# Performance work log

Measured on AMD Instinct MI355X. Metric: run time of the kernel, lower is better.

## Reference

```python
import jax, jax.numpy as jnp
import numpy as np

NEG_SLOPE = 0.01  # torch leaky_relu default


def kan_linear(x, coeffs, bias):
    """Fourier KAN linear. x: [..., I], coeffs: [2, O, I, G], bias: [O] or None."""
    G = coeffs.shape[-1]
    k = jnp.arange(1, G + 1, dtype=x.dtype)            # [G]
    xb = x[..., None] * k                               # [..., I, G]
    y = jnp.einsum('...ig,oig->...o', jnp.cos(xb), coeffs[0]) \
      + jnp.einsum('...ig,oig->...o', jnp.sin(xb), coeffs[1])
    if bias is not None:
        y = y + bias
    return y


def setup_inputs() -> dict:
    key = jax.random.key(0)
    N, E = 50000, 500000
    IN, IE, FN, FE, H, G = 128, 64, 128, 32, 4, 4
    D = IN + IE
    HFE, HFN = H * FE, H * FN
    ks = jax.random.split(key, 16)
    def nrm(k, shape, scale):
        return jax.random.normal(k, shape, dtype=jnp.float32) * scale
    return {
        'node_feats': nrm(ks[0], (N, IN), 1.0),
        'edge_feats': nrm(ks[1], (E, IE), 1.0),
        'src': jax.random.randint(ks[2], (E,), 0, N, dtype=jnp.int32),
        'dst': jax.random.randint(ks[3], (E,), 0, N, dtype=jnp.int32),
        'W_ni': nrm(ks[4], (IN, HFE), 0.05),
        'W_nj': nrm(ks[5], (IN, HFE), 0.05),
        'W_fij': nrm(ks[6], (IE, HFE), 0.05),
        'W_node': nrm(ks[7], (D, HFN), 0.05),
        'b_node': jnp.zeros((HFN,), jnp.float32),
        'attn': nrm(ks[8], (H, FE), 0.1),
        'bias_edge': jnp.zeros((HFE,), jnp.float32),
        'ek_c': nrm(ks[9], (2, HFE, HFE, 1), 1.0 / np.sqrt(HFE)),
        'ek_b': jnp.zeros((HFE,), jnp.float32),
        'nk_c': nrm(ks[10], (2, D, D, 1), 1.0 / np.sqrt(D)),
        'nk_b': jnp.zeros((D,), jnp.float32),
        'on_c': nrm(ks[11], (2, FN, FN, G), 1.0 / np.sqrt(FN * G)),
        'on_b': jnp.zeros((FN,), jnp.float32),
        'oe_c': nrm(ks[12], (2, FE, FE, G), 1.0 / np.sqrt(FE * G)),
        'oe_b': jnp.zeros((FE,), jnp.float32),
    }


def reference(node_feats, edge_feats, src, dst, W_ni, W_nj, W_fij, W_node, b_node,
              attn, bias_edge, ek_c, ek_b, nk_c, nk_b, on_c, on_b, oe_c, oe_b):
    N = node_feats.shape[0]
    H, FE = attn.shape

    # edge feature path: f_ni[u] + f_nj[v] + f_fij -> KAN -> bias -> leaky_relu
    f = (node_feats @ W_ni)[src] + (node_feats @ W_nj)[dst] + edge_feats @ W_fij  # [E, H*FE]
    f = kan_linear(f, ek_c, ek_b) + bias_edge
    f = jax.nn.leaky_relu(f, NEG_SLOPE)
    f = f.reshape(-1, H, FE)                                  # [E, H, FE]

    # attention scores + edge softmax over incoming edges of dst
    scores = jnp.sum(f * attn, axis=-1)                        # [E, H]
    smax = jax.ops.segment_max(scores, dst, num_segments=N)    # [N, H]
    e = jnp.exp(scores - smax[dst])
    ssum = jax.ops.segment_sum(e, dst, num_segments=N)
    a = e / ssum[dst]                                          # [E, H]

    # mean aggregation of raw edge feats onto dst nodes
    ones = jnp.ones((src.shape[0],), node_feats.dtype)
    deg = jax.ops.segment_sum(ones, dst, num_segments=N)       # [N]
    agg = jax.ops.segment_sum(edge_feats, dst, num_segments=N) / jnp.maximum(deg, 1.0)[:, None]

    merged = jnp.concatenate([node_feats, agg], axis=1)        # [N, IN+IE]
    merged = kan_linear(merged, nk_c, nk_b)

    h = (merged @ W_node + b_node).reshape(N, H, -1)           # [N, H, FN]
    m = h[src] * a[:, :, None]                                 # [E, H, FN]
    h_out = jax.ops.segment_sum(m, dst, num_segments=N)        # [N, H, FN]
    h_out = jnp.sum(jax.nn.leaky_relu(h_out, NEG_SLOPE), axis=1)  # [N, FN]

    f_sum = jnp.sum(f, axis=1)                                 # [E, FE]
    out_node = kan_linear(h_out, on_c, on_b)                   # [N, FN]
    out_edge = kan_linear(f_sum, oe_c, oe_b)                   # [E, FE]
    return out_node, out_edge
```

## Files before the change

### kernel.cpp

```cpp
#include <hip/hip_runtime.h>
#include <hip/hip_bf16.h>
#include <math.h>

#define NEG 0.01f

typedef __attribute__((ext_vector_type(8))) short short8;
typedef __attribute__((ext_vector_type(4))) float f32x4;
typedef unsigned short ushort;

#define MFMA(a,b,c) __builtin_amdgcn_mfma_f32_16x16x32_bf16(a,b,c,0,0,0)

__device__ __forceinline__ float leaky(float x){ return x >= 0.f ? x : NEG*x; }
__device__ __forceinline__ ushort b16(float f){
  unsigned int u = __float_as_uint(f);
  unsigned int r = (u + 0x7FFF + ((u >> 16) & 1)) >> 16;
  return (ushort)r;
}

__global__ void k_deg(const int* __restrict__ dst, int* __restrict__ deg, int E){
  int e = blockIdx.x*256 + threadIdx.x;
  if (e < E) atomicAdd(&deg[dst[e]], 1);
}

__global__ __launch_bounds__(1024) void k_scan(const int* __restrict__ deg, int* __restrict__ off, int N){
  __shared__ int buf[1024];
  __shared__ int carry_s;
  if (threadIdx.x == 0) carry_s = 0;
  __syncthreads();
  for (int base = 0; base < N; base += 1024){
    int i = base + threadIdx.x;
    int v = (i < N) ? deg[i] : 0;
    buf[threadIdx.x] = v;
    __syncthreads();
    for (int s = 1; s < 1024; s <<= 1){
      int t = (threadIdx.x >= s) ? buf[threadIdx.x - s] : 0;
      __syncthreads();
      buf[threadIdx.x] += t;
      __syncthreads();
    }
    if (i < N) off[i] = carry_s + buf[threadIdx.x] - v;
    int tot = buf[1023];
    __syncthreads();
    if (threadIdx.x == 0) carry_s += tot;
    __syncthreads();
  }
  if (threadIdx.x == 0) off[N] = carry_s;
}

__global__ void k_fill(const int* __restrict__ dst, const int* __restrict__ off,
                       int* __restrict__ cursor, int* __restrict__ eids, int E){
  int e = blockIdx.x*256 + threadIdx.x;
  if (e < E){
    int d = dst[e];
    int p = atomicAdd(&cursor[d], 1);
    eids[off[d] + p] = e;
  }
}

__global__ void k_prep2(const float* __restrict__ W_ni, const float* __restrict__ W_nj,
                        const float* __restrict__ W_fij, const float* __restrict__ W_node,
                        const float* __restrict__ ek_c, const float* __restrict__ nk_c,
                        const float* __restrict__ on_c, const float* __restrict__ oe_c,
                        ushort* __restrict__ Bni, ushort* __restrict__ Bnj,
                        ushort* __restrict__ Bfij, ushort* __restrict__ BE,
                        ushort* __restrict__ BN_, ushort* __restrict__ BW,
                        ushort* __restrict__ BO, ushort* __restrict__ BOE){
  int t = blockIdx.x*256 + threadIdx.x;
  if (t < 16384){ int o = t >> 7, i = t & 127; Bni[t] = b16(W_ni[i*128 + o]); return; }
  t -= 16384;
  if (t < 16384){ int o = t >> 7, i = t & 127; Bnj[t] = b16(W_nj[i*128 + o]); return; }
  t -= 16384;
  if (t < 8192){ int o = t >> 6, i = t & 63; Bfij[t] = b16(W_fij[i*128 + o]); return; }
  t -= 8192;
  if (t < 32768){ int o = t >> 8, k = t & 255; int tt = k >> 7, i = k & 127;
    BE[t] = b16(ek_c[((tt*128 + o) << 7) + i]); return; }
  t -= 32768;
  if (t < 73728){ int o = t / 384, k = t % 384; int tt = (k >= 192), i = k - tt*192;
    BN_[t] = b16(nk_c[(tt*192 + o)*192 + i]); return; }
  t -= 73728;
  if (t < 98304){ int o = t / 192, i = t % 192; BW[t] = b16(W_node[i*512 + o]); return; }
  t -= 98304;
  if (t < 131072){ int o = t >> 10, k = t & 1023; int tt = k >> 9, q = k & 511, i = q >> 2, g = q & 3;
    BO[t] = b16(on_c[(((tt*128 + o) << 7) + i)*4 + g]); return; }
  t -= 131072;
  if (t < 8192){ int o = t >> 8, k = t & 255; int tt = k >> 7, q = k & 127, i = q >> 2, g = q & 3;
    BOE[t] = b16(oe_c[((tt*32 + o)*32 + i)*4 + g]); return; }
}

template<int MODE>
__global__ __launch_bounds__(256) void k_mm(
    const float* __restrict__ A, int lda, const float* __restrict__ A2,
    const ushort* __restrict__ B,
    float* __restrict__ C, int ldc, const float* __restrict__ bias,
    int M, int K)
{
  __shared__ __align__(16) ushort As[64*40];
  const int tid = threadIdx.x;
  const int lane = tid & 63, w = tid >> 6;
  const int l15 = lane & 15, kg = lane >> 4;
  const int r0 = blockIdx.x * 64;
  const int c0 = blockIdx.y * 64;
  const int rg = (w & 1) * 2;
  const int cgb = (w >> 1) * 2;
  f32x4 acc[2][2] = {};
  const int srow = tid >> 2;
  const int kk = (tid & 3) * 8;

  for (int k0 = 0; k0 < K; k0 += 32){
    {
      int row = r0 + srow;
      ushort v[8];
      if (MODE == 0){
        if (row < M){
          const float* p = A + (size_t)row*lda + k0 + kk;
          float4 a = *(const float4*)p, b = *(const float4*)(p+4);
          v[0]=b16(a.x); v[1]=b16(a.y); v[2]=b16(a.z); v[3]=b16(a.w);
          v[4]=b16(b.x); v[5]=b16(b.y); v[6]=b16(b.z); v[7]=b16(b.w);
        } else { for (int j=0;j<8;j++) v[j]=0; }
      } else if (MODE == 1){
        int k = k0 + kk;
        int tt = k >> 9, i = (k & 511) >> 2;
        float x0 = 0.f, x1 = 0.f;
        if (row < M){ x0 = A[(size_t)row*128 + i]; x1 = A[(size_t)row*128 + i + 1]; }
        #pragma unroll
        for (int g = 1; g <= 4; g++){
          v[g-1]   = b16(tt ? __sinf(x0*(float)g) : __cosf(x0*(float)g));
          v[3+g]   = b16(tt ? __sinf(x1*(float)g) : __cosf(x1*(float)g));
        }
      } else {
        int k = k0 + kk;
        int tt = (k >= 192), i = k - tt*192;
        float xv8[8] = {0,0,0,0,0,0,0,0};
        if (row < M){
          const float* sp = (i < 128) ? (A + (size_t)row*128 + i) : (A2 + (size_t)row*64 + (i - 128));
          float4 a = *(const float4*)sp, b = *(const float4*)(sp+4);
          xv8[0]=a.x; xv8[1]=a.y; xv8[2]=a.z; xv8[3]=a.w;
          xv8[4]=b.x; xv8[5]=b.y; xv8[6]=b.z; xv8[7]=b.w;
        }
        #pragma unroll
        for (int j = 0; j < 8; j++)
          v[j] = b16(tt ? __sinf(xv8[j]) : __cosf(xv8[j]));
      }
      *(short8*)&As[srow*40 + kk] = *(short8*)v;
    }
    __syncthreads();
    short8 afr[2], bfr[2];
    #pragma unroll
    for (int q = 0; q < 2; q++)
      afr[q] = *(const short8*)&As[((rg+q)*16 + l15)*40 + kg*8];
    #pragma unroll
    for (int q = 0; q < 2; q++)
      bfr[q] = *(const short8*)(B + (size_t)(c0 + (cgb+q)*16 + l15)*K + k0 + kg*8);
    #pragma unroll
    for (int i = 0; i < 2; i++)
      #pragma unroll
      for (int j = 0; j < 2; j++)
        acc[i][j] = MFMA(afr[i], bfr[j], acc[i][j]);
    __syncthreads();
  }
  #pragma unroll
  for (int i = 0; i < 2; i++){
    #pragma unroll
    for (int j = 0; j < 2; j++){
      int col = c0 + (cgb+j)*16 + l15;
      float bv = bias ? bias[col] : 0.f;
      #pragma unroll
      for (int r = 0; r < 4; r++){
        int row = r0 + (rg+i)*16 + kg*4 + r;
        if (row < M) C[(size_t)row*ldc + col] = acc[i][j][r] + bv;
      }
    }
  }
}

__global__ __launch_bounds__(256) void k_edge(
    const float* __restrict__ P,
    const float* __restrict__ ef,
    const int* __restrict__ src, const int* __restrict__ dst,
    const ushort* __restrict__ Bfij,
    const ushort* __restrict__ BE,
    const ushort* __restrict__ BOE,
    const float* __restrict__ ek_b, const float* __restrict__ bias_edge,
    const float* __restrict__ attn, const float* __restrict__ oe_b,
    float* __restrict__ scores,
    float* __restrict__ out_edge,
    int E)
{
  __shared__ __align__(16) ushort cs[32*264];
  __shared__ float fsum[32*33];
  __shared__ float attn_s[128], ekb_s[128], oeb_s[32];
  __shared__ int se[32], de[32];
  const int tid = threadIdx.x;
  const int lane = tid & 63, w = tid >> 6;
  const int l15 = lane & 15, kg = lane >> 4;
  const int e0 = blockIdx.x << 5;

  if (tid < 128){ attn_s[tid] = attn[tid]; ekb_s[tid] = ek_b[tid] + bias_edge[tid]; }
  if (tid < 32){ oeb_s[tid] = oe_b[tid]; se[tid] = src[e0+tid]; de[tid] = dst[e0+tid]; }
  __syncthreads();

  const int eg = w & 1, cq = w >> 1;

  short8 afe[2];
  #pragma unroll
  for (int ks = 0; ks < 2; ks++){
    const float* p = ef + (size_t)(e0 + eg*16 + l15)*64 + ks*32 + kg*8;
    float4 u0 = *(const float4*)p, u1 = *(const float4*)(p+4);
    ushort tv[8] = {b16(u0.x),b16(u0.y),b16(u0.z),b16(u0.w),b16(u1.x),b16(u1.y),b16(u1.z),b16(u1.w)};
    afe[ks] = *(short8*)tv;
  }
  float xv[4][4];
  #pragma unroll
  for (int cg = 0; cg < 4; cg++){
    int c = (cq*4 + cg)*16;
    f32x4 acc = {0.f,0.f,0.f,0.f};
    #pragma unroll
    for (int ks = 0; ks < 2; ks++){
      short8 bf = *(const short8*)(Bfij + (size_t)(c + l15)*64 + ks*32 + kg*8);
      acc = MFMA(afe[ks], bf, acc);
    }
    int col = c + l15;
    #pragma unroll
    for (int r = 0; r < 4; r++){
      int e = eg*16 + kg*4 + r;
      xv[cg][r] = acc[r] + P[(size_t)se[e]*256 + col] + P[(size_t)de[e]*256 + 128 + col];
    }
  }
  #pragma unroll
  for (int cg = 0; cg < 4; cg++){
    int col = (cq*4 + cg)*16 + l15;
    #pragma unroll
    for (int r = 0; r < 4; r++){
      int e = eg*16 + kg*4 + r;
      cs[e*264 + col]       = b16(__cosf(xv[cg][r]));
      cs[e*264 + 128 + col] = b16(__sinf(xv[cg][r]));
    }
  }
  __syncthreads();

  short8 af[8];
  #pragma unroll
  for (int ks = 0; ks < 8; ks++)
    af[ks] = *(const short8*)&cs[(eg*16 + l15)*264 + ks*32 + kg*8];
  float fv[4][4];
  #pragma unroll
  for (int cg = 0; cg < 4; cg++){
    int c = (cq*4 + cg)*16;
    f32x4 acc = {0.f,0.f,0.f,0.f};
    #pragma unroll
    for (int ks = 0; ks < 8; ks++){
      short8 bf = *(const short8*)(BE + (size_t)(c + l15)*256 + ks*32 + kg*8);
      acc = MFMA(af[ks], bf, acc);
    }
    int col = c + l15;
    #pragma unroll
    for (int r = 0; r < 4; r++)
      fv[cg][r] = leaky(acc[r] + ekb_s[col]);
  }
  __syncthreads();
  float* f_lds = (float*)cs;
  #pragma unroll
  for (int cg = 0; cg < 4; cg++){
    int col = (cq*4 + cg)*16 + l15;
    #pragma unroll
    for (int r = 0; r < 4; r++)
      f_lds[(eg*16 + kg*4 + r)*132 + col] = fv[cg][r];
  }
  __syncthreads();

  if (tid < 128){
    int e = tid >> 2, h = tid & 3;
    float s = 0.f;
    #pragma unroll
    for (int j = 0; j < 32; j++) s += f_lds[e*132 + h*32 + j] * attn_s[h*32 + j];
    scores[(size_t)(e0 + e)*4 + h] = s;
  }
  {
    int e = tid >> 3, j0 = (tid & 7)*4;
    #pragma unroll
    for (int j2 = 0; j2 < 4; j2++){
      int j = j0 + j2;
      fsum[e*33 + j] = f_lds[e*132 + j] + f_lds[e*132 + 32 + j]
                     + f_lds[e*132 + 64 + j] + f_lds[e*132 + 96 + j];
    }
  }
  __syncthreads();

  {
    int e = tid >> 3, i0 = (tid & 7)*4;
    ushort cb[16], sb[16];
    #pragma unroll
    for (int i2 = 0; i2 < 4; i2++){
      float x = fsum[e*33 + i0 + i2];
      #pragma unroll
      for (int g = 1; g <= 4; g++){
        float xg = x * (float)g;
        cb[i2*4 + g - 1] = b16(__cosf(xg));
        sb[i2*4 + g - 1] = b16(__sinf(xg));
      }
    }
    *(short8*)&cs[e*264 + i0*4]           = ((short8*)cb)[0];
    *(short8*)&cs[e*264 + i0*4 + 8]       = ((short8*)cb)[1];
    *(short8*)&cs[e*264 + 128 + i0*4]     = ((short8*)sb)[0];
    *(short8*)&cs[e*264 + 128 + i0*4 + 8] = ((short8*)sb)[1];
  }
  __syncthreads();

  {
    int eg5 = w & 1, cg5 = w >> 1;
    f32x4 acc = {0.f,0.f,0.f,0.f};
    #pragma unroll
    for (int ks = 0; ks < 8; ks++){
      short8 a  = *(const short8*)&cs[(eg5*16 + l15)*264 + ks*32 + kg*8];
      short8 bf = *(const short8*)(BOE + (size_t)(cg5*16 + l15)*256 + ks*32 + kg*8);
      acc = MFMA(a, bf, acc);
    }
    int col = cg5*16 + l15;
    #pragma unroll
    for (int r = 0; r < 4; r++){
      int e = eg5*16 + kg*4 + r;
      out_edge[(size_t)(e0 + e)*32 + col] = acc[r] + oeb_s[col];
    }
  }
}

__global__ __launch_bounds__(256) void k_nodestats(
    const float* __restrict__ edge_feats, const float* __restrict__ scores,
    const int* __restrict__ off, const int* __restrict__ eids,
    float* __restrict__ agg, float* __restrict__ smax, float* __restrict__ rssum, int N)
{
  int n = blockIdx.x*4 + (threadIdx.x >> 6);
  int lane = threadIdx.x & 63;
  if (n >= N) return;
  int s0 = off[n], s1 = off[n+1], d = s1 - s0;
  float acc = 0.f;
  for (int t = s0; t < s1; t++){
    int eid = eids[t];
    acc += edge_feats[(size_t)eid*64 + lane];
  }
  agg[(size_t)n*64 + lane] = acc / (float)max(d, 1);
  if (lane < 4){
    float m = -1e30f;
    for (int t = s0; t < s1; t++) m = fmaxf(m, scores[(size_t)eids[t]*4 + lane]);
    float ss = 0.f;
    for (int t = s0; t < s1; t++) ss += __expf(scores[(size_t)eids[t]*4 + lane] - m);
    smax[n*4 + lane]  = (d > 0) ? m : 0.f;
    rssum[n*4 + lane] = (d > 0) ? 1.f/ss : 0.f;
  }
}

__global__ __launch_bounds__(256) void k_aggr(
    const float* __restrict__ h,
    const float* __restrict__ scores,
    const int* __restrict__ src,
    const int* __restrict__ off, const int* __restrict__ eids,
    const float* __restrict__ smax, const float* __restrict__ rssum,
    float* __restrict__ h_out, int N)
{
  __shared__ float part[256];
  int n = blockIdx.x;
  int tid = threadIdx.x;
  int ha = tid >> 7;
  int s0 = off[n], s1 = off[n+1];
  float ma = smax[n*4 + ha],  mb = smax[n*4 + ha + 2];
  float ra = rssum[n*4 + ha], rb = rssum[n*4 + ha + 2];
  float acc_a = 0.f, acc_b = 0.f;
  for (int t = s0; t < s1; t++){
    int eid = eids[t];
    int sv = src[eid];
    float aa = __expf(scores[(size_t)eid*4 + ha]     - ma) * ra;
    float ab = __expf(scores[(size_t)eid*4 + ha + 2] - mb) * rb;
    acc_a += aa * h[(size_t)sv*512 + tid];
    acc_b += ab * h[(size_t)sv*512 + 256 + tid];
  }
  part[tid] = leaky(acc_a) + leaky(acc_b);
  __syncthreads();
  if (tid < 128) h_out[(size_t)n*128 + tid] = part[tid] + part[tid + 128];
}

extern "C" void kernel_launch(void* const* d_in, const int* in_sizes, int n_in,
                              void* d_out, int out_size, void* d_ws, size_t ws_size,
                              hipStream_t stream){
  const float* node_feats = (const float*)d_in[0];
  const float* edge_feats = (const float*)d_in[1];
  const int*   src        = (const int*)  d_in[2];
  const int*   dst        = (const int*)  d_in[3];
  const float* W_ni       = (const float*)d_in[4];
  const float* W_nj       = (const float*)d_in[5];
  const float* W_fij      = (const float*)d_in[6];
  const float* W_node     = (const float*)d_in[7];
  const float* b_node     = (const float*)d_in[8];
  const float* attn       = (const float*)d_in[9];
  const float* bias_edge  = (const float*)d_in[10];
  const float* ek_c       = (const float*)d_in[11];
  const float* ek_b       = (const float*)d_in[12];
  const float* nk_c       = (const float*)d_in[13];
  const float* nk_b       = (const float*)d_in[14];
  const float* on_c       = (const float*)d_in[15];
  const float* on_b       = (const float*)d_in[16];
  const float* oe_c       = (const float*)d_in[17];
  const float* oe_b       = (const float*)d_in[18];

  const int N = in_sizes[0] / 128;
  const int E = in_sizes[2];

  float* ws = (float*)d_ws;
  size_t o = 0;
  float* P      = ws + o; o += (size_t)N*256;
  float* scores = ws + o; o += (size_t)E*4;
  float* smax   = ws + o; o += (size_t)N*4;
  float* rssum  = ws + o; o += (size_t)N*4;
  float* agg    = ws + o; o += (size_t)N*64;
  float* mk     = ws + o; o += (size_t)N*192;
  float* h      = ws + o; o += (size_t)N*512;
  float* h_out  = ws + o; o += (size_t)N*128;
  o = (o + 7) & ~(size_t)7;
  ushort* Bni  = (ushort*)(ws + o); o += 8192;
  ushort* Bnj  = (ushort*)(ws + o); o += 8192;
  ushort* Bfij = (ushort*)(ws + o); o += 4096;
  ushort* BE   = (ushort*)(ws + o); o += 16384;
  ushort* BN_  = (ushort*)(ws + o); o += 36864;
  ushort* BW   = (ushort*)(ws + o); o += 49152;
  ushort* BO   = (ushort*)(ws + o); o += 65536;
  ushort* BOE  = (ushort*)(ws + o); o += 4096;
  int* deg    = (int*)(ws + o); o += N;
  int* cursor = (int*)(ws + o); o += N;
  int* off    = (int*)(ws + o); o += (size_t)(N + 1);
  int* eids   = (int*)(ws + o); o += E;

  float* out_node = (float*)d_out;
  float* out_edge = (float*)d_out + (size_t)N*128;

  (void)hipMemsetAsync(deg, 0, sizeof(int)*(size_t)(2*N), stream);

  k_deg <<<(E + 255)/256, 256, 0, stream>>>(dst, deg, E);
  k_scan<<<1, 1024, 0, stream>>>(deg, off, N);
  k_fill<<<(E + 255)/256, 256, 0, stream>>>(dst, off, cursor, eids, E);
  k_prep2<<<1505, 256, 0, stream>>>(W_ni, W_nj, W_fij, W_node, ek_c, nk_c, on_c, oe_c,
                                    Bni, Bnj, Bfij, BE, BN_, BW, BO, BOE);

  const int MB = (N + 63)/64;
  k_mm<0><<<dim3(MB, 2), 256, 0, stream>>>(node_feats, 128, nullptr, Bni, P,       256, nullptr, N, 128);
  k_mm<0><<<dim3(MB, 2), 256, 0, stream>>>(node_feats, 128, nullptr, Bnj, P + 128, 256, nullptr, N, 128);

  k_edge<<<E/32, 256, 0, stream>>>(P, edge_feats, src, dst, Bfij, BE, BOE,
                                   ek_b, bias_edge, attn, oe_b, scores, out_edge, E);

  k_nodestats<<<(N + 3)/4, 256, 0, stream>>>(edge_feats, scores, off, eids, agg, smax, rssum, N);

  k_mm<2><<<dim3(MB, 3), 256, 0, stream>>>(node_feats, 128, agg, BN_, mk, 192, nk_b, N, 384);
  k_mm<0><<<dim3(MB, 8), 256, 0, stream>>>(mk, 192, nullptr, BW, h, 512, b_node, N, 192);

  k_aggr<<<N, 256, 0, stream>>>(h, scores, src, off, eids, smax, rssum, h_out, N);

  k_mm<1><<<dim3(MB, 2), 256, 0, stream>>>(h_out, 128, nullptr, BO, out_node, 128, on_b, N, 1024);
}
```

Before: 1.077 ms.

## Restructure edge kernel per-wave, precompute attention alphas, parallelize scan

Rewrites the edge kernel so each wave owns 16 edges and computes all 128 columns itself. Intermediate results stay in registers and per-wave LDS, which removes block-wide barriers, and the scores come from shuffle reductions. Other changes: a new kernel precomputes softmax alphas once per edge-head so the aggregation loop avoids redundant exp work, the scan runs over chunks in parallel instead of serial 1024-wide passes, the two P GEMMs merge into one launch, and setprio hints wrap the MFMA sections. The risks are higher register pressure in the edge kernel and an extra pass writing alpha, which reuses the P buffer.

New measurement: 1.154 ms. 1.07x slower.

```diff
diff --git a/kernel.cpp b/kernel.cpp
--- a/kernel.cpp
+++ b/kernel.cpp
@@ -16,6 +16,12 @@
   unsigned int r = (u + 0x7FFF + ((u >> 16) & 1)) >> 16;
   return (ushort)r;
 }
+__device__ __forceinline__ short8 pack8(const float* f){
+  union { ushort s[8]; short8 v; } t;
+  #pragma unroll
+  for (int j = 0; j < 8; j++) t.s[j] = b16(f[j]);
+  return t.v;
+}
 
 __global__ void k_deg(const int* __restrict__ dst, int* __restrict__ deg, int E){
   int e = blockIdx.x*256 + threadIdx.x;
@@ -23,28 +29,29 @@
 }
 
 __global__ __launch_bounds__(1024) void k_scan(const int* __restrict__ deg, int* __restrict__ off, int N){
-  __shared__ int buf[1024];
-  __shared__ int carry_s;
-  if (threadIdx.x == 0) carry_s = 0;
+  __shared__ int sums[1024];
+  int tid = threadIdx.x;
+  int per = (N + 1023) / 1024;
+  int s0 = tid * per;
+  int local = 0;
+  for (int i = 0; i < per; i++){
+    int idx = s0 + i;
+    if (idx < N) local += deg[idx];
+  }
+  sums[tid] = local;
   __syncthreads();
-  for (int base = 0; base < N; base += 1024){
-    int i = base + threadIdx.x;
-    int v = (i < N) ? deg[i] : 0;
-    buf[threadIdx.x] = v;
+  for (int s = 1; s < 1024; s <<= 1){
+    int t = (tid >= s) ? sums[tid - s] : 0;
     __syncthreads();
-    for (int s = 1; s < 1024; s <<= 1){
-      int t = (threadIdx.x >= s) ? buf[threadIdx.x - s] : 0;
-      __syncthreads();
-      buf[threadIdx.x] += t;
-      __syncthreads();
-    }
-    if (i < N) off[i] = carry_s + buf[threadIdx.x] - v;
-    int tot = buf[1023];
+    sums[tid] += t;
     __syncthreads();
-    if (threadIdx.x == 0) carry_s += tot;
-    __syncthreads();
-  }
-  if (threadIdx.x == 0) off[N] = carry_s;
+  }
+  int run = sums[tid] - local;
+  for (int i = 0; i < per; i++){
+    int idx = s0 + i;
+    if (idx < N){ off[idx] = run; run += deg[idx]; }
+  }
+  if (tid == 1023) off[N] = run;
 }
 
 __global__ void k_fill(const int* __restrict__ dst, const int* __restrict__ off,
@@ -109,14 +116,14 @@
   for (int k0 = 0; k0 < K; k0 += 32){
     {
       int row = r0 + srow;
-      ushort v[8];
+      float v[8];
       if (MODE == 0){
         if (row < M){
           const float* p = A + (size_t)row*lda + k0 + kk;
           float4 a = *(const float4*)p, b = *(const float4*)(p+4);
-          v[0]=b16(a.x); v[1]=b16(a.y); v[2]=b16(a.z); v[3]=b16(a.w);
-          v[4]=b16(b.x); v[5]=b16(b.y); v[6]=b16(b.z); v[7]=b16(b.w);
-        } else { for (int j=0;j<8;j++) v[j]=0; }
+          v[0]=a.x; v[1]=a.y; v[2]=a.z; v[3]=a.w;
+          v[4]=b.x; v[5]=b.y; v[6]=b.z; v[7]=b.w;
+        } else { for (int j=0;j<8;j++) v[j]=0.f; }
       } else if (MODE == 1){
         int k = k0 + kk;
         int tt = k >> 9, i = (k & 511) >> 2;
@@ -124,8 +131,8 @@
         if (row < M){ x0 = A[(size_t)row*128 + i]; x1 = A[(size_t)row*128 + i + 1]; }
         #pragma unroll
         for (int g = 1; g <= 4; g++){
-          v[g-1]   = b16(tt ? __sinf(x0*(float)g) : __cosf(x0*(float)g));
-          v[3+g]   = b16(tt ? __sinf(x1*(float)g) : __cosf(x1*(float)g));
+          v[g-1] = tt ? __sinf(x0*(float)g) : __cosf(x0*(float)g);
+          v[3+g] = tt ? __sinf(x1*(float)g) : __cosf(x1*(float)g);
         }
       } else {
         int k = k0 + kk;
@@ -139,9 +146,11 @@
         }
         #pragma unroll
         for (int j = 0; j < 8; j++)
-          v[j] = b16(tt ? __sinf(xv8[j]) : __cosf(xv8[j]));
+          xv8[j] = tt ? __sinf(xv8[j]) : __cosf(xv8[j]);
+        #pragma unroll
+        for (int j = 0; j < 8; j++) v[j] = xv8[j];
       }
-      *(short8*)&As[srow*40 + kk] = *(short8*)v;
+      *(short8*)&As[srow*40 + kk] = pack8(v);
     }
     __syncthreads();
     short8 afr[2], bfr[2];
@@ -186,142 +195,163 @@
     float* __restrict__ out_edge,
     int E)
 {
-  __shared__ __align__(16) ushort cs[32*264];
-  __shared__ float fsum[32*33];
-  __shared__ float attn_s[128], ekb_s[128], oeb_s[32];
-  __shared__ int se[32], de[32];
+  __shared__ __align__(16) float shmem[4*2112];
   const int tid = threadIdx.x;
   const int lane = tid & 63, w = tid >> 6;
   const int l15 = lane & 15, kg = lane >> 4;
-  const int e0 = blockIdx.x << 5;
-
-  if (tid < 128){ attn_s[tid] = attn[tid]; ekb_s[tid] = ek_b[tid] + bias_edge[tid]; }
-  if (tid < 32){ oeb_s[tid] = oe_b[tid]; se[tid] = src[e0+tid]; de[tid] = dst[e0+tid]; }
-  __syncthreads();
-
-  const int eg = w & 1, cq = w >> 1;
-
+  const int e0 = (blockIdx.x*4 + w) * 16;
+  if (e0 >= E) return;
+  float* xw  = shmem + w*2112;
+  float* fsw = xw;
+
+  int sr[4], dr[4];
+  #pragma unroll
+  for (int r = 0; r < 4; r++){ sr[r] = src[e0 + kg*4 + r]; dr[r] = dst[e0 + kg*4 + r]; }
+  float attnv[8], ekbv[8];
+  #pragma unroll
+  for (int cg = 0; cg < 8; cg++){
+    int col = cg*16 + l15;
+    attnv[cg] = attn[col];
+    ekbv[cg]  = ek_b[col] + bias_edge[col];
+  }
+  float oebv[2] = { oe_b[l15], oe_b[16 + l15] };
+
+  f32x4 acc[8];
+  #pragma unroll
+  for (int cg = 0; cg < 8; cg++){
+    int col = cg*16 + l15;
+    #pragma unroll
+    for (int r = 0; r < 4; r++)
+      acc[cg][r] = P[(size_t)sr[r]*256 + col] + P[(size_t)dr[r]*256 + 128 + col];
+  }
   short8 afe[2];
   #pragma unroll
   for (int ks = 0; ks < 2; ks++){
-    const float* p = ef + (size_t)(e0 + eg*16 + l15)*64 + ks*32 + kg*8;
+    const float* p = ef + (size_t)(e0 + l15)*64 + ks*32 + kg*8;
     float4 u0 = *(const float4*)p, u1 = *(const float4*)(p+4);
-    ushort tv[8] = {b16(u0.x),b16(u0.y),b16(u0.z),b16(u0.w),b16(u1.x),b16(u1.y),b16(u1.z),b16(u1.w)};
-    afe[ks] = *(short8*)tv;
-  }
-  float xv[4][4];
-  #pragma unroll
-  for (int cg = 0; cg < 4; cg++){
-    int c = (cq*4 + cg)*16;
-    f32x4 acc = {0.f,0.f,0.f,0.f};
+    float tv[8] = {u0.x,u0.y,u0.z,u0.w,u1.x,u1.y,u1.z,u1.w};
+    afe[ks] = pack8(tv);
+  }
+  __builtin_amdgcn_s_setprio(1);
+  #pragma unroll
+  for (int cg = 0; cg < 8; cg++){
     #pragma unroll
     for (int ks = 0; ks < 2; ks++){
-      short8 bf = *(const short8*)(Bfij + (size_t)(c + l15)*64 + ks*32 + kg*8);
-      acc = MFMA(afe[ks], bf, acc);
-    }
-    int col = c + l15;
-    #pragma unroll
-    for (int r = 0; r < 4; r++){
-      int e = eg*16 + kg*4 + r;
-      xv[cg][r] = acc[r] + P[(size_t)se[e]*256 + col] + P[(size_t)de[e]*256 + 128 + col];
-    }
-  }
-  #pragma unroll
-  for (int cg = 0; cg < 4; cg++){
-    int col = (cq*4 + cg)*16 + l15;
-    #pragma unroll
-    for (int r = 0; r < 4; r++){
-      int e = eg*16 + kg*4 + r;
-      cs[e*264 + col]       = b16(__cosf(xv[cg][r]));
-      cs[e*264 + 128 + col] = b16(__sinf(xv[cg][r]));
-    }
-  }
-  __syncthreads();
-
-  short8 af[8];
-  #pragma unroll
-  for (int ks = 0; ks < 8; ks++)
-    af[ks] = *(const short8*)&cs[(eg*16 + l15)*264 + ks*32 + kg*8];
-  float fv[4][4];
-  #pragma unroll
-  for (int cg = 0; cg < 4; cg++){
-    int c = (cq*4 + cg)*16;
-    f32x4 acc = {0.f,0.f,0.f,0.f};
+      short8 bf = *(const short8*)(Bfij + (size_t)(cg*16 + l15)*64 + ks*32 + kg*8);
+      acc[cg] = MFMA(afe[ks], bf, acc[cg]);
+    }
+  }
+  __builtin_amdgcn_s_setprio(0);
+  #pragma unroll
+  for (int cg = 0; cg < 8; cg++)
+    #pragma unroll
+    for (int r = 0; r < 4; r++)
+      xw[(kg*4 + r)*132 + cg*16 + l15] = acc[cg][r];
+  __builtin_amdgcn_sched_barrier(0);
+
+  float xv[4][8];
+  #pragma unroll
+  for (int s = 0; s < 4; s++){
+    float4 q0 = *(const float4*)&xw[l15*132 + s*32 + kg*8];
+    float4 q1 = *(const float4*)&xw[l15*132 + s*32 + kg*8 + 4];
+    xv[s][0]=q0.x; xv[s][1]=q0.y; xv[s][2]=q0.z; xv[s][3]=q0.w;
+    xv[s][4]=q1.x; xv[s][5]=q1.y; xv[s][6]=q1.z; xv[s][7]=q1.w;
+  }
+  short8 afr[8];
+  #pragma unroll
+  for (int s = 0; s < 4; s++){
+    float tc[8], ts[8];
+    #pragma unroll
+    for (int j = 0; j < 8; j++){ tc[j] = __cosf(xv[s][j]); ts[j] = __sinf(xv[s][j]); }
+    afr[s]     = pack8(tc);
+    afr[s + 4] = pack8(ts);
+  }
+  f32x4 facc[8];
+  __builtin_amdgcn_s_setprio(1);
+  #pragma unroll
+  for (int cg = 0; cg < 8; cg++){
+    f32x4 a = { ekbv[cg], ekbv[cg], ekbv[cg], ekbv[cg] };
     #pragma unroll
     for (int ks = 0; ks < 8; ks++){
-      short8 bf = *(const short8*)(BE + (size_t)(c + l15)*256 + ks*32 + kg*8);
-      acc = MFMA(af[ks], bf, acc);
-    }
-    int col = c + l15;
+      short8 bf = *(const short8*)(BE + (size_t)(cg*16 + l15)*256 + ks*32 + kg*8);
+      a = MFMA(afr[ks], bf, a);
+    }
+    facc[cg] = a;
+  }
+  __builtin_amdgcn_s_setprio(0);
+  float fv[8][4];
+  #pragma unroll
+  for (int cg = 0; cg < 8; cg++)
     #pragma unroll
     for (int r = 0; r < 4; r++)
-      fv[cg][r] = leaky(acc[r] + ekb_s[col]);
-  }
-  __syncthreads();
-  float* f_lds = (float*)cs;
-  #pragma unroll
-  for (int cg = 0; cg < 4; cg++){
-    int col = (cq*4 + cg)*16 + l15;
+      fv[cg][r] = leaky(facc[cg][r]);
+
+  float p[4][4] = {};
+  #pragma unroll
+  for (int cg = 0; cg < 8; cg++){
+    int hh = cg >> 1;
+    #pragma unroll
+    for (int r = 0; r < 4; r++) p[hh][r] += fv[cg][r] * attnv[cg];
+  }
+  #pragma unroll
+  for (int m = 1; m <= 8; m <<= 1)
+    #pragma unroll
+    for (int hh = 0; hh < 4; hh++)
+      #pragma unroll
+      for (int r = 0; r < 4; r++)
+        p[hh][r] += __shfl_xor(p[hh][r], m, 64);
+  {
+    float outv = 0.f;
+    #pragma unroll
+    for (int hh = 0; hh < 4; hh++)
+      #pragma unroll
+      for (int rr = 0; rr < 4; rr++)
+        if (l15 == hh*4 + rr) outv = p[hh][rr];
+    scores[(size_t)(e0 + kg*4 + (l15 & 3))*4 + (l15 >> 2)] = outv;
+  }
+
+  #pragma unroll
+  for (int c2 = 0; c2 < 2; c2++)
     #pragma unroll
     for (int r = 0; r < 4; r++)
-      f_lds[(eg*16 + kg*4 + r)*132 + col] = fv[cg][r];
-  }
-  __syncthreads();
-
-  if (tid < 128){
-    int e = tid >> 2, h = tid & 3;
-    float s = 0.f;
-    #pragma unroll
-    for (int j = 0; j < 32; j++) s += f_lds[e*132 + h*32 + j] * attn_s[h*32 + j];
-    scores[(size_t)(e0 + e)*4 + h] = s;
-  }
-  {
-    int e = tid >> 3, j0 = (tid & 7)*4;
-    #pragma unroll
-    for (int j2 = 0; j2 < 4; j2++){
-      int j = j0 + j2;
-      fsum[e*33 + j] = f_lds[e*132 + j] + f_lds[e*132 + 32 + j]
-                     + f_lds[e*132 + 64 + j] + f_lds[e*132 + 96 + j];
-    }
-  }
-  __syncthreads();
-
-  {
-    int e = tid >> 3, i0 = (tid & 7)*4;
-    ushort cb[16], sb[16];
-    #pragma unroll
-    for (int i2 = 0; i2 < 4; i2++){
-      float x = fsum[e*33 + i0 + i2];
-      #pragma unroll
-      for (int g = 1; g <= 4; g++){
-        float xg = x * (float)g;
-        cb[i2*4 + g - 1] = b16(__cosf(xg));
-        sb[i2*4 + g - 1] = b16(__sinf(xg));
-      }
-    }
-    *(short8*)&cs[e*264 + i0*4]           = ((short8*)cb)[0];
-    *(short8*)&cs[e*264 + i0*4 + 8]       = ((short8*)cb)[1];
-    *(short8*)&cs[e*264 + 128 + i0*4]     = ((short8*)sb)[0];
-    *(short8*)&cs[e*264 + 128 + i0*4 + 8] = ((short8*)sb)[1];
-  }
-  __syncthreads();
-
-  {
-    int eg5 = w & 1, cg5 = w >> 1;
-    f32x4 acc = {0.f,0.f,0.f,0.f};
+      fsw[(kg*4 + r)*36 + c2*16 + l15] = fv[c2][r] + fv[c2+2][r] + fv[c2+4][r] + fv[c2+6][r];
+  __builtin_amdgcn_sched_barrier(0);
+
+  float2 fsp[4];
+  #pragma unroll
+  for (int a = 0; a < 4; a++)
+    fsp[a] = *(const float2*)&fsw[l15*36 + a*8 + kg*2];
+  short8 afr5[8];
+  #pragma unroll
+  for (int ks = 0; ks < 8; ks++){
+    int a = ks & 3;
+    float tv[8];
+    #pragma unroll
+    for (int j = 0; j < 8; j++){
+      float base = (j < 4) ? fsp[a].x : fsp[a].y;
+      float xg = base * (float)((j & 3) + 1);
+      tv[j] = (ks < 4) ? __cosf(xg) : __sinf(xg);
+    }
+    afr5[ks] = pack8(tv);
+  }
+  f32x4 oacc[2];
+  __builtin_amdgcn_s_setprio(1);
+  #pragma unroll
+  for (int cg5 = 0; cg5 < 2; cg5++){
+    f32x4 a = { oebv[cg5], oebv[cg5], oebv[cg5], oebv[cg5] };
     #pragma unroll
     for (int ks = 0; ks < 8; ks++){
-      short8 a  = *(const short8*)&cs[(eg5*16 + l15)*264 + ks*32 + kg*8];
       short8 bf = *(const short8*)(BOE + (size_t)(cg5*16 + l15)*256 + ks*32 + kg*8);
-      acc = MFMA(a, bf, acc);
-    }
-    int col = cg5*16 + l15;
-    #pragma unroll
-    for (int r = 0; r < 4; r++){
-      int e = eg5*16 + kg*4 + r;
-      out_edge[(size_t)(e0 + e)*32 + col] = acc[r] + oeb_s[col];
-    }
-  }
+      a = MFMA(afr5[ks], bf, a);
+    }
+    oacc[cg5] = a;
+  }
+  __builtin_amdgcn_s_setprio(0);
+  #pragma unroll
+  for (int cg5 = 0; cg5 < 2; cg5++)
+    #pragma unroll
+    for (int r = 0; r < 4; r++)
+      out_edge[(size_t)(e0 + kg*4 + r)*32 + cg5*16 + l15] = oacc[cg5][r];
 }
 
 __global__ __launch_bounds__(256) void k_nodestats(
@@ -349,12 +379,22 @@
   }
 }
 
+__global__ void k_alpha(const float* __restrict__ scores, const int* __restrict__ dst,
+                        const float* __restrict__ smax, const float* __restrict__ rssum,
+                        float* __restrict__ alpha, int M){
+  int t = blockIdx.x*256 + threadIdx.x;
+  if (t < M){
+    int e = t >> 2, hh = t & 3;
+    int d = dst[e];
+    alpha[t] = __expf(scores[t] - smax[d*4 + hh]) * rssum[d*4 + hh];
+  }
+}
+
 __global__ __launch_bounds__(256) void k_aggr(
     const float* __restrict__ h,
-    const float* __restrict__ scores,
+    const float* __restrict__ alpha,
     const int* __restrict__ src,
     const int* __restrict__ off, const int* __restrict__ eids,
-    const float* __restrict__ smax, const float* __restrict__ rssum,
     float* __restrict__ h_out, int N)
 {
   __shared__ float part[256];
@@ -362,14 +402,12 @@
   int tid = threadIdx.x;
   int ha = tid >> 7;
   int s0 = off[n], s1 = off[n+1];
-  float ma = smax[n*4 + ha],  mb = smax[n*4 + ha + 2];
-  float ra = rssum[n*4 + ha], rb = rssum[n*4 + ha + 2];
   float acc_a = 0.f, acc_b = 0.f;
   for (int t = s0; t < s1; t++){
     int eid = eids[t];
     int sv = src[eid];
-    float aa = __expf(scores[(size_t)eid*4 + ha]     - ma) * ra;
-    float ab = __expf(scores[(size_t)eid*4 + ha + 2] - mb) * rb;
+    float aa = alpha[(size_t)eid*4 + ha];
+    float ab = alpha[(size_t)eid*4 + ha + 2];
     acc_a += aa * h[(size_t)sv*512 + tid];
     acc_b += ab * h[(size_t)sv*512 + 256 + tid];
   }
@@ -428,6 +466,8 @@
   int* off    = (int*)(ws + o); o += (size_t)(N + 1);
   int* eids   = (int*)(ws + o); o += E;
 
+  float* alpha = P;
+
   float* out_node = (float*)d_out;
   float* out_edge = (float*)d_out + (size_t)N*128;
 
@@ -440,18 +480,18 @@
                                     Bni, Bnj, Bfij, BE, BN_, BW, BO, BOE);
 
   const int MB = (N + 63)/64;
-  k_mm<0><<<dim3(MB, 2), 256, 0, stream>>>(node_feats, 128, nullptr, Bni, P,       256, nullptr, N, 128);
-  k_mm<0><<<dim3(MB, 2), 256, 0, stream>>>(node_feats, 128, nullptr, Bnj, P + 128, 256, nullptr, N, 128);
-
-  k_edge<<<E/32, 256, 0, stream>>>(P, edge_feats, src, dst, Bfij, BE, BOE,
-                                   ek_b, bias_edge, attn, oe_b, scores, out_edge, E);
+  k_mm<0><<<dim3(MB, 4), 256, 0, stream>>>(node_feats, 128, nullptr, Bni, P, 256, nullptr, N, 128);
+
+  k_edge<<<(E + 63)/64, 256, 0, stream>>>(P, edge_feats, src, dst, Bfij, BE, BOE,
+                                          ek_b, bias_edge, attn, oe_b, scores, out_edge, E);
 
   k_nodestats<<<(N + 3)/4, 256, 0, stream>>>(edge_feats, scores, off, eids, agg, smax, rssum, N);
+  k_alpha<<<(E*4 + 255)/256, 256, 0, stream>>>(scores, dst, smax, rssum, alpha, E*4);
 
   k_mm<2><<<dim3(MB, 3), 256, 0, stream>>>(node_feats, 128, agg, BN_, mk, 192, nk_b, N, 384);
   k_mm<0><<<dim3(MB, 8), 256, 0, stream>>>(mk, 192, nullptr, BW, h, 512, b_node, N, 192);
 
-  k_aggr<<<N, 256, 0, stream>>>(h, scores, src, off, eids, smax, rssum, h_out, N);
+  k_aggr<<<N, 256, 0, stream>>>(h, alpha, src, off, eids, h_out, N);
 
   k_mm<1><<<dim3(MB, 2), 256, 0, stream>>>(h_out, 128, nullptr, BO, out_node, 128, on_b, N, 1024);
 }
```
